# Kernel tuning notes

Measured on AMD Instinct MI355X. Metric: run time of the kernel, lower is better.

Reference implementation:

```python
import jax, jax.numpy as jnp
import numpy as np

# ---- multi-res 4D hash encoding config (Instant-NGP style) ----
L = 16                     # num_levels
T = 2 ** 19                # hash table entries per level (log2_hashmap_size)
FDIM = 2                   # features per entry (input_ch = L*2)
MIN_RES = np.array([16, 16, 16, 16], dtype=np.float64)
MAX_RES = np.array([256, 256, 256, 128], dtype=np.float64)
_growth = (MAX_RES / MIN_RES) ** (1.0 / (L - 1))
RES = np.floor(MIN_RES[None, :] * _growth[None, :] ** np.arange(L)[:, None]).astype(np.int32)  # [L,4]
PRIMES = np.array([1, 2654435761, 805459861, 3674653429], dtype=np.uint32)
# 16 corner offsets of the 4D hypercube
OFFS = np.array([[(c >> d) & 1 for d in range(4)] for c in range(16)], dtype=np.int32)  # [16,4]


def hash_encode(x, table):
    """x: [N,4] in [0,1); table: [L,T,FDIM] -> [N, L*FDIM]."""
    offs = jnp.asarray(OFFS)
    primes = jnp.asarray(PRIMES)
    outs = []
    for l in range(L):  # fixed small loop over levels
        res = jnp.asarray(RES[l], dtype=x.dtype)          # [4]
        pos = x * (res - 1.0)                              # [N,4]
        base = jnp.floor(pos)
        frac = pos - base                                  # [N,4]
        base_i = base.astype(jnp.int32)
        coord = jnp.clip(base_i[:, None, :] + offs[None], 0, jnp.asarray(RES[l] - 1))  # [N,16,4]
        h = coord.astype(jnp.uint32) * primes              # [N,16,4] u32 wraparound mult
        idx = (h[..., 0] ^ h[..., 1] ^ h[..., 2] ^ h[..., 3]) & jnp.uint32(T - 1)      # [N,16]
        feats = table[l][idx.astype(jnp.int32)]            # irregular gather -> [N,16,FDIM]
        # quadrilinear weights: prod over dims of frac / (1-frac)
        w = jnp.prod(jnp.where(offs[None] == 1, frac[:, None, :], 1.0 - frac[:, None, :]), axis=-1)  # [N,16]
        outs.append(jnp.einsum('nc,ncf->nf', w, feats))    # [N,FDIM]
    return jnp.concatenate(outs, axis=-1)                  # [N, L*FDIM]


def setup_inputs() -> dict:
    key = jax.random.key(0)
    ks = jax.random.split(key, 8)
    N = 1048576
    H = 64
    in_ch = L * FDIM  # 32
    x = jax.random.uniform(ks[0], (N, 4), dtype=jnp.float32)
    # NGP hash tables initialized uniform in [-1e-4, 1e-4]
    table = jax.random.uniform(ks[1], (L, T, FDIM), dtype=jnp.float32, minval=-1e-4, maxval=1e-4)
    def lin(k, out_d, in_d):
        b = 1.0 / np.sqrt(in_d)
        return jax.random.uniform(k, (out_d, in_d), dtype=jnp.float32, minval=-b, maxval=b)
    w0 = lin(ks[2], H, in_ch)
    w1 = lin(ks[3], H, H)
    w2 = lin(ks[4], H, H)
    w_out = lin(ks[5], 3, H)
    b_out = jax.random.uniform(ks[6], (3,), dtype=jnp.float32, minval=-1.0/np.sqrt(H), maxval=1.0/np.sqrt(H))
    return {"x": x, "table": table, "w0": w0, "w1": w1, "w2": w2, "w_out": w_out, "b_out": b_out}


def reference(x, table, w0, w1, w2, w_out, b_out):
    h = hash_encode(x, table)                 # [N, 32]
    for W in (w0, w1, w2):                    # bias-free Linear + ReLU x3
        h = jax.nn.relu(h @ W.T)
    v = h @ w_out.T + b_out                   # [N, 3]
    return v
```

## Files before the change

### kernel.cpp

```cpp
#include <hip/hip_runtime.h>
#include <math.h>

#define NLVL  16
#define TSZ   (1u << 19)
#define TMASK (TSZ - 1u)

struct ResArr { int m1[NLVL * 4]; };

typedef short  short8  __attribute__((ext_vector_type(8)));
typedef float  float4v __attribute__((ext_vector_type(4)));

static __device__ __forceinline__ unsigned short f2bf(float f) {
    unsigned u = __float_as_uint(f);
    return (unsigned short)((u + 0x7fffu + ((u >> 16) & 1u)) >> 16);
}

__global__ __launch_bounds__(256)
void cvt_table(const float4* __restrict__ t, uint2* __restrict__ o, int totalPairs)
{
    for (int i = blockIdx.x * 256 + (int)threadIdx.x; i < totalPairs;
         i += gridDim.x * 256) {
        const float4 e = t[i];
        o[i] = make_uint2((unsigned)f2bf(e.x) | ((unsigned)f2bf(e.y) << 16),
                          (unsigned)f2bf(e.z) | ((unsigned)f2bf(e.w) << 16));
    }
}

static __device__ __forceinline__
void encode_point_bf16(const float4*   __restrict__ x,
                       const unsigned* __restrict__ tbl,
                       unsigned*       __restrict__ featbf,
                       int N, int l, int n, const ResArr& res)
{
    if (n >= N) return;

    const float4 xv = x[n];
    const float px[4] = {xv.x, xv.y, xv.z, xv.w};

    int   bi[4];
    float fr[4], om[4];
    #pragma unroll
    for (int d = 0; d < 4; ++d) {
        const int r = res.m1[l * 4 + d];
        const float pos = px[d] * (float)r;
        const float fb  = floorf(pos);
        fr[d] = pos - fb;
        om[d] = 1.0f - fr[d];
        bi[d] = (int)fb;
    }
    const unsigned* tl  = tbl + (size_t)l * TSZ;
    const uint2*    tl2 = (const uint2*)tl;
    const uint4*    tl4 = (const uint4*)tl;

    unsigned hrest[8];
    #pragma unroll
    for (int p = 0; p < 8; ++p) {
        const int c1 = bi[1] + ( p       & 1);
        const int c2 = bi[2] + ((p >> 1) & 1);
        const int c3 = bi[3] + ((p >> 2) & 1);
        hrest[p] = ((unsigned)c1 * 2654435761u)
                 ^ ((unsigned)c2 * 805459861u)
                 ^ ((unsigned)c3 * 3674653429u);
    }

    const int b0 = bi[0];
    unsigned ea[8], eb[8];

    if ((b0 & 1) == 0) {
        #pragma unroll
        for (int p = 0; p < 8; ++p) {
            const unsigned h = ((unsigned)b0 ^ hrest[p]) & TMASK;
            const uint2 q = tl2[h >> 1];
            ea[p] = (h & 1u) ? q.y : q.x;
            eb[p] = (h & 1u) ? q.x : q.y;
        }
    } else if ((b0 & 3) == 1) {
        #pragma unroll
        for (int p = 0; p < 8; ++p) {
            const unsigned hA = ((unsigned)b0 ^ hrest[p]) & TMASK;
            const uint4 q = tl4[hA >> 2];
            const unsigned jA  = hA & 3u;
            const unsigned loA = (jA & 2u) ? q.z : q.x;
            const unsigned hiA = (jA & 2u) ? q.w : q.y;
            const unsigned loB = (jA & 2u) ? q.x : q.z;
            const unsigned hiB = (jA & 2u) ? q.y : q.w;
            ea[p] = (jA & 1u) ? hiA : loA;
            eb[p] = (jA & 1u) ? loB : hiB;
        }
    } else {
        #pragma unroll
        for (int p = 0; p < 8; ++p) {
            const unsigned hA = ((unsigned)b0       ^ hrest[p]) & TMASK;
            const unsigned hB = ((unsigned)(b0 + 1) ^ hrest[p]) & TMASK;
            ea[p] = tl[hA];
            eb[p] = tl[hB];
        }
    }

    float2 fv[16];
    #pragma unroll
    for (int p = 0; p < 8; ++p) {
        fv[2 * p]     = make_float2(__uint_as_float(ea[p] << 16),
                                    __uint_as_float(ea[p] & 0xffff0000u));
        fv[2 * p + 1] = make_float2(__uint_as_float(eb[p] << 16),
                                    __uint_as_float(eb[p] & 0xffff0000u));
    }

    float wt[16];
    #pragma unroll
    for (int c = 0; c < 16; ++c) {
        float w = ( c       & 1) ? fr[0] : om[0];
        w      *= ((c >> 1) & 1) ? fr[1] : om[1];
        w      *= ((c >> 2) & 1) ? fr[2] : om[2];
        w      *= ((c >> 3) & 1) ? fr[3] : om[3];
        wt[c] = w;
    }

    float a0 = 0.0f, a1 = 0.0f;
    #pragma unroll
    for (int c = 0; c < 16; ++c) {
        a0 = fmaf(wt[c], fv[c].x, a0);
        a1 = fmaf(wt[c], fv[c].y, a1);
    }
    featbf[(size_t)l * N + n] = (unsigned)f2bf(a0) | ((unsigned)f2bf(a1) << 16);
}

__global__ __launch_bounds__(256, 4)
void ingp_encode_bf16(const float4*   __restrict__ x,
                      const unsigned* __restrict__ tbl,
                      unsigned*       __restrict__ featbf,
                      int N, int chunksPerLevel, ResArr res)
{
    const int l     = blockIdx.x / chunksPerLevel;
    const int chunk = blockIdx.x - l * chunksPerLevel;
    encode_point_bf16(x, tbl, featbf, N, l, chunk * 256 + (int)threadIdx.x, res);
}

static __device__ __forceinline__
void encode_point_f32(const float4* __restrict__ x,
                      const float2* __restrict__ table,
                      unsigned*     __restrict__ featbf,
                      int N, int l, int n, const ResArr& res)
{
    if (n >= N) return;

    const float4 xv = x[n];
    const float px[4] = {xv.x, xv.y, xv.z, xv.w};

    int   bi[4];
    float fr[4], om[4];
    #pragma unroll
    for (int d = 0; d < 4; ++d) {
        const int r = res.m1[l * 4 + d];
        const float pos = px[d] * (float)r;
        const float fb  = floorf(pos);
        fr[d] = pos - fb;
        om[d] = 1.0f - fr[d];
        bi[d] = (int)fb;
    }
    const float2* tl  = table + (size_t)l * TSZ;
    const float4* tl4 = (const float4*)tl;

    unsigned hrest[8];
    #pragma unroll
    for (int p = 0; p < 8; ++p) {
        const int c1 = bi[1] + ( p       & 1);
        const int c2 = bi[2] + ((p >> 1) & 1);
        const int c3 = bi[3] + ((p >> 2) & 1);
        hrest[p] = ((unsigned)c1 * 2654435761u)
                 ^ ((unsigned)c2 * 805459861u)
                 ^ ((unsigned)c3 * 3674653429u);
    }

    float2 fv[16];
    if ((bi[0] & 1) == 0) {
        #pragma unroll
        for (int p = 0; p < 8; ++p) {
            const unsigned h = ((unsigned)bi[0] ^ hrest[p]) & TMASK;
            const float4 q = tl4[h >> 1];
            const bool odd = (h & 1);
            fv[2 * p]     = odd ? make_float2(q.z, q.w) : make_float2(q.x, q.y);
            fv[2 * p + 1] = odd ? make_float2(q.x, q.y) : make_float2(q.z, q.w);
        }
    } else {
        #pragma unroll
        for (int p = 0; p < 8; ++p) {
            const unsigned hA = ((unsigned)bi[0]       ^ hrest[p]) & TMASK;
            const unsigned hB = ((unsigned)(bi[0] + 1) ^ hrest[p]) & TMASK;
            fv[2 * p]     = tl[hA];
            fv[2 * p + 1] = tl[hB];
        }
    }

    float wt[16];
    #pragma unroll
    for (int c = 0; c < 16; ++c) {
        float w = ( c       & 1) ? fr[0] : om[0];
        w      *= ((c >> 1) & 1) ? fr[1] : om[1];
        w      *= ((c >> 2) & 1) ? fr[2] : om[2];
        w      *= ((c >> 3) & 1) ? fr[3] : om[3];
        wt[c] = w;
    }

    float a0 = 0.0f, a1 = 0.0f;
    #pragma unroll
    for (int c = 0; c < 16; ++c) {
        a0 = fmaf(wt[c], fv[c].x, a0);
        a1 = fmaf(wt[c], fv[c].y, a1);
    }
    featbf[(size_t)l * N + n] = (unsigned)f2bf(a0) | ((unsigned)f2bf(a1) << 16);
}

__global__ __launch_bounds__(256, 4)
void ingp_encode_f32(const float4* __restrict__ x,
                     const float2* __restrict__ table,
                     unsigned*     __restrict__ featbf,
                     int N, int chunksPerLevel, ResArr res)
{
    const int l     = blockIdx.x / chunksPerLevel;
    const int chunk = blockIdx.x - l * chunksPerLevel;
    encode_point_f32(x, table, featbf, N, l, chunk * 256 + (int)threadIdx.x, res);
}

#define TILE_BODY(P0, A0)                                                     \
{                                                                             \
    asm volatile("" : "+v"(idx0));    \
    float4v acc0[4];                                                          \
    _Pragma("unroll")                                                         \
    for (int t = 0; t < 4; ++t) {                                             \
        acc0[t] = (float4v){0.f, 0.f, 0.f, 0.f};                              \
        acc0[t] = __builtin_amdgcn_mfma_f32_16x16x32_bf16(A0, w0f[t], acc0[t], 0, 0, 0); \
    }                                                                         \
    _Pragma("unroll")                                                         \
    for (int t = 0; t < 4; ++t)                                               \
        _Pragma("unroll")                                                     \
        for (int r = 0; r < 4; ++r)                                           \
            *(unsigned short*)(hbase + (q * 4 + r) * 144 + (t * 16 + nn) * 2) = \
                f2bf(fmaxf(acc0[t][r], 0.0f));                                \
    short8 a1[2];                                                             \
    _Pragma("unroll")                                                         \
    for (int s = 0; s < 2; ++s)                                               \
        a1[s] = *(const short8*)(hbase + nn * 144 + s * 64 + q * 16);         \
    float4v acc1[4];                                                          \
    _Pragma("unroll")                                                         \
    for (int t = 0; t < 4; ++t) {                                             \
        acc1[t] = (float4v){0.f, 0.f, 0.f, 0.f};                              \
        _Pragma("unroll")                                                     \
        for (int s = 0; s < 2; ++s)                                           \
            acc1[t] = __builtin_amdgcn_mfma_f32_16x16x32_bf16(a1[s], w1f[s][t], acc1[t], 0, 0, 0); \
    }                                                                         \
    _Pragma("unroll")                                                         \
    for (int t = 0; t < 4; ++t)                                               \
        _Pragma("unroll")                                                     \
        for (int r = 0; r < 4; ++r)                                           \
            *(unsigned short*)(hbase + (q * 4 + r) * 144 + (t * 16 + nn) * 2) = \
                f2bf(fmaxf(acc1[t][r], 0.0f));                                \
    short8 a2[2];                                                             \
    _Pragma("unroll")                                                         \
    for (int s = 0; s < 2; ++s)                                               \
        a2[s] = *(const short8*)(hbase + nn * 144 + s * 64 + q * 16);         \
    float4v acc2[4];                                                          \
    _Pragma("unroll")                                                         \
    for (int t = 0; t < 4; ++t) {                                             \
        acc2[t] = (float4v){0.f, 0.f, 0.f, 0.f};                              \
        _Pragma("unroll")                                                     \
        for (int s = 0; s < 2; ++s) {                                         \
            const short8 w2x = *(const short8*)(wlds + ((12 + s * 4 + t) * 64 + lane) * 16 + idx0); \
            acc2[t] = __builtin_amdgcn_mfma_f32_16x16x32_bf16(a2[s], w2x, acc2[t], 0, 0, 0); \
        }                                                                     \
    }                                                                         \
    _Pragma("unroll")                                                         \
    for (int t = 0; t < 4; ++t)                                               \
        _Pragma("unroll")                                                     \
        for (int r = 0; r < 4; ++r)                                           \
            *(unsigned short*)(hbase + (q * 4 + r) * 144 + (t * 16 + nn) * 2) = \
                f2bf(fmaxf(acc2[t][r], 0.0f));                                \
    short8 a3[2];                                                             \
    _Pragma("unroll")                                                         \
    for (int s = 0; s < 2; ++s)                                               \
        a3[s] = *(const short8*)(hbase + nn * 144 + s * 64 + q * 16);         \
    float4v oc = (float4v){0.f, 0.f, 0.f, 0.f};                               \
    _Pragma("unroll")                                                         \
    for (int s = 0; s < 2; ++s) {                                             \
        const short8 wox = *(const short8*)(wlds + ((20 + s) * 64 + lane) * 16 + idx0); \
        oc = __builtin_amdgcn_mfma_f32_16x16x32_bf16(a3[s], wox, oc, 0, 0, 0); \
    }                                                                         \
    if (nn < 3) {                                                             \
        _Pragma("unroll")                                                     \
        for (int r = 0; r < 4; ++r) {                                         \
            const int pt = (P0) + q * 4 + r;                                  \
            if (pt < N) out[pt * 3 + nn] = oc[r] + bias;                      \
        }                                                                     \
    }                                                                         \
}

static __device__ __forceinline__
void stage_wlds(const float* __restrict__ w0, const float* __restrict__ w1,
                const float* __restrict__ w2, const float* __restrict__ wout,
                char* wlds, int tid)
{
    if (tid < 64) {
        const int lane = tid;
        const int q  = lane >> 4;
        const int nn = lane & 15;
        #pragma unroll
        for (int t = 0; t < 4; ++t) {
            const float* wr = w0 + (t * 16 + nn) * 32 + q * 8;
            short8 f;
            #pragma unroll
            for (int e = 0; e < 8; ++e) f[e] = (short)f2bf(wr[e]);
            *(short8*)(wlds + ((0 + t) * 64 + lane) * 16) = f;
        }
        #pragma unroll
        for (int s = 0; s < 2; ++s)
            #pragma unroll
            for (int t = 0; t < 4; ++t) {
                const float* wr1 = w1 + (t * 16 + nn) * 64 + s * 32 + q * 8;
                const float* wr2 = w2 + (t * 16 + nn) * 64 + s * 32 + q * 8;
                short8 f1, f2;
                #pragma unroll
                for (int e = 0; e < 8; ++e) {
                    f1[e] = (short)f2bf(wr1[e]);
                    f2[e] = (short)f2bf(wr2[e]);
                }
                *(short8*)(wlds + (( 4 + s * 4 + t) * 64 + lane) * 16) = f1;
                *(short8*)(wlds + ((12 + s * 4 + t) * 64 + lane) * 16) = f2;
            }
        #pragma unroll
        for (int s = 0; s < 2; ++s) {
            short8 f;
            #pragma unroll
            for (int e = 0; e < 8; ++e)
                f[e] = (nn < 3) ? (short)f2bf(wout[nn * 64 + s * 32 + q * 8 + e])
                                : (short)0;
            *(short8*)(wlds + ((20 + s) * 64 + lane) * 16) = f;
        }
    }
}

template <int NT>
static __device__ __forceinline__
void mlp_run(const unsigned* __restrict__ featbf,
             const float*    __restrict__ bout,
             float*          __restrict__ out,
             const char* wlds, char* hbase,
             int N, int firstTile, int lane)
{
    const int q  = lane >> 4;
    const int nn = lane & 15;

    short8 w0f[4];
    #pragma unroll
    for (int t = 0; t < 4; ++t)
        w0f[t] = *(const short8*)(wlds + ((0 + t) * 64 + lane) * 16);
    short8 w1f[2][4];
    #pragma unroll
    for (int s = 0; s < 2; ++s)
        #pragma unroll
        for (int t = 0; t < 4; ++t)
            w1f[s][t] = *(const short8*)(wlds + ((4 + s * 4 + t) * 64 + lane) * 16);
    const float bias = (nn < 3) ? bout[nn] : 0.0f;

    int idx0 = 0;

    unsigned ufA[4], ufB[4];
    {
        const int pA = (firstTile * 16 < N) ? (firstTile * 16 + nn) : 0;
        const int pB = ((firstTile + 1) * 16 < N) ? ((firstTile + 1) * 16 + nn) : 0;
        #pragma unroll
        for (int v = 0; v < 4; ++v) {
            ufA[v] = featbf[(size_t)(q * 4 + v) * N + pA];
            ufB[v] = featbf[(size_t)(q * 4 + v) * N + pB];
        }
    }

    for (int it = 0; it < NT; it += 2) {
        const int p0A = (firstTile + it) * 16;
        if (p0A >= N) break;

        short8 a0A;
        #pragma unroll
        for (int v = 0; v < 4; ++v) {
            a0A[2 * v]     = (short)(ufA[v] & 0xffffu);
            a0A[2 * v + 1] = (short)(ufA[v] >> 16);
        }
        {
            const int p0n = (firstTile + it + 2) * 16;
            const bool more = (it + 2 < NT) && (p0n < N);
            const int pn = more ? (p0n + nn) : 0;
            #pragma unroll
            for (int v = 0; v < 4; ++v)
                ufA[v] = featbf[(size_t)(q * 4 + v) * N + pn];
        }
        TILE_BODY(p0A, a0A)

        const int p0B = (firstTile + it + 1) * 16;
        if (p0B < N && it + 1 < NT) {
            short8 a0B;
            #pragma unroll
            for (int v = 0; v < 4; ++v) {
                a0B[2 * v]     = (short)(ufB[v] & 0xffffu);
                a0B[2 * v + 1] = (short)(ufB[v] >> 16);
            }
            {
                const int p0n = (firstTile + it + 3) * 16;
                const bool more = (it + 3 < NT) && (p0n < N);
                const int pn = more ? (p0n + nn) : 0;
                #pragma unroll
                for (int v = 0; v < 4; ++v)
                    ufB[v] = featbf[(size_t)(q * 4 + v) * N + pn];
            }
            TILE_BODY(p0B, a0B)
        }
    }
}

#define TILES_PER_WAVE 16

__global__ __launch_bounds__(256, 4)
void ingp_mlp_mfma(const unsigned* __restrict__ featbf,
                   const float*    __restrict__ w0,
                   const float*    __restrict__ w1,
                   const float*    __restrict__ w2,
                   const float*    __restrict__ wout,
                   const float*    __restrict__ bout,
                   float*          __restrict__ out,
                   int N)
{
    __shared__ char lds_raw[4 * 16 * 144];
    __shared__ char wlds[22 * 64 * 16];

    const int tid = (int)threadIdx.x;
    stage_wlds(w0, w1, w2, wout, wlds, tid);
    __syncthreads();

    const int wave = tid >> 6;
    const int lane = tid & 63;
    char* hbase = lds_raw + wave * (16 * 144);
    mlp_run<TILES_PER_WAVE>(featbf, bout, out, wlds, hbase, N,
                            ((int)blockIdx.x * 4 + wave) * TILES_PER_WAVE, lane);
}

__global__ __launch_bounds__(256, 2)
void ingp_fused(const float4* __restrict__ x,
                const float2* __restrict__ table,
                const float*  __restrict__ w0,
                const float*  __restrict__ w1,
                const float*  __restrict__ w2,
                const float*  __restrict__ wout,
                const float*  __restrict__ bout,
                float*        __restrict__ out,
                int N, ResArr res)
{
    const int n = blockIdx.x * blockDim.x + threadIdx.x;
    if (n >= N) return;

    const float4 xv = x[n];
    const float px[4] = {xv.x, xv.y, xv.z, xv.w};

    float h1[64];
    #pragma unroll
    for (int j = 0; j < 64; ++j) h1[j] = 0.0f;

    float a0p = 0.0f, a1p = 0.0f;

    #pragma unroll 1
    for (int l = 0; l < NLVL; ++l) {
        int   rm[4], bi[4];
        float fr[4], om[4];
        #pragma unroll
        for (int d = 0; d < 4; ++d) {
            const int r = res.m1[l * 4 + d];
            rm[d] = r;
            const float pos = px[d] * (float)r;
            const float fb  = floorf(pos);
            fr[d] = pos - fb;
            om[d] = 1.0f - fr[d];
            bi[d] = (int)fb;
        }
        const float2* tl = table + (size_t)l * TSZ;

        float2 fv[16];
        float  wt[16];
        #pragma unroll
        for (int c = 0; c < 16; ++c) {
            int c0 = bi[0] + ( c       & 1);
            int c1 = bi[1] + ((c >> 1) & 1);
            int c2 = bi[2] + ((c >> 2) & 1);
            int c3 = bi[3] + ((c >> 3) & 1);
            c0 = min(max(c0, 0), rm[0]);
            c1 = min(max(c1, 0), rm[1]);
            c2 = min(max(c2, 0), rm[2]);
            c3 = min(max(c3, 0), rm[3]);
            const unsigned hh = (unsigned)c0
                              ^ ((unsigned)c1 * 2654435761u)
                              ^ ((unsigned)c2 * 805459861u)
                              ^ ((unsigned)c3 * 3674653429u);
            fv[c] = tl[hh & TMASK];
            float w = ( c       & 1) ? fr[0] : om[0];
            w      *= ((c >> 1) & 1) ? fr[1] : om[1];
            w      *= ((c >> 2) & 1) ? fr[2] : om[2];
            w      *= ((c >> 3) & 1) ? fr[3] : om[3];
            wt[c] = w;
        }
        {
            const int lp = (l == 0) ? 0 : (l - 1);
            const float* w0c = w0 + 2 * lp;
            #pragma unroll
            for (int j = 0; j < 64; ++j)
                h1[j] = fmaf(w0c[j * 32], a0p, fmaf(w0c[j * 32 + 1], a1p, h1[j]));
        }
        float a0 = 0.0f, a1 = 0.0f;
        #pragma unroll
        for (int c = 0; c < 16; ++c) {
            a0 = fmaf(wt[c], fv[c].x, a0);
            a1 = fmaf(wt[c], fv[c].y, a1);
        }
        a0p = a0; a1p = a1;
    }
    {
        const float* w0c = w0 + 2 * (NLVL - 1);
        #pragma unroll
        for (int j = 0; j < 64; ++j)
            h1[j] = fmaf(w0c[j * 32], a0p, fmaf(w0c[j * 32 + 1], a1p, h1[j]));
    }
    #pragma unroll
    for (int j = 0; j < 64; ++j) h1[j] = fmaxf(h1[j], 0.0f);

    float h2[64];
    #pragma unroll
    for (int j = 0; j < 64; ++j) {
        float acc = 0.0f;
        const float* wr = w1 + j * 64;
        #pragma unroll
        for (int i = 0; i < 64; ++i) acc = fmaf(wr[i], h1[i], acc);
        h2[j] = fmaxf(acc, 0.0f);
    }
    float h3[64];
    #pragma unroll
    for (int j = 0; j < 64; ++j) {
        float acc = 0.0f;
        const float* wr = w2 + j * 64;
        #pragma unroll
        for (int i = 0; i < 64; ++i) acc = fmaf(wr[i], h2[i], acc);
        h3[j] = fmaxf(acc, 0.0f);
    }
    float o[3];
    #pragma unroll
    for (int k = 0; k < 3; ++k) {
        float acc = bout[k];
        const float* wr = wout + k * 64;
        #pragma unroll
        for (int i = 0; i < 64; ++i) acc = fmaf(wr[i], h3[i], acc);
        o[k] = acc;
    }
    out[n * 3 + 0] = o[0];
    out[n * 3 + 1] = o[1];
    out[n * 3 + 2] = o[2];
}

extern "C" void kernel_launch(void* const* d_in, const int* in_sizes, int n_in,
                              void* d_out, int out_size, void* d_ws, size_t ws_size,
                              hipStream_t stream) {
    (void)n_in; (void)out_size;

    const float* x     = (const float*)d_in[0];
    const float* table = (const float*)d_in[1];
    const float* w0    = (const float*)d_in[2];
    const float* w1    = (const float*)d_in[3];
    const float* w2    = (const float*)d_in[4];
    const float* wout  = (const float*)d_in[5];
    const float* bout  = (const float*)d_in[6];
    float* out = (float*)d_out;

    const int N = in_sizes[0] / 4;

    ResArr res;
    for (int d = 0; d < 4; ++d) {
        const double minr = 16.0;
        const double maxr = (d == 3) ? 128.0 : 256.0;
        const double growth = pow(maxr / minr, 1.0 / (double)(NLVL - 1));
        for (int l = 0; l < NLVL; ++l) {
            const int r = (int)floor(minr * pow(growth, (double)l));
            res.m1[l * 4 + d] = r - 1;
        }
    }

    const size_t tblBytes  = (size_t)NLVL * TSZ * sizeof(unsigned);
    const size_t featBytes = (size_t)NLVL * (size_t)N * sizeof(unsigned);
    const int chunksPerLevel = (N + 255) / 256;

    const int tiles  = (N + 15) / 16;
    const int waves  = (tiles + TILES_PER_WAVE - 1) / TILES_PER_WAVE;
    const int blocks = (waves + 3) / 4;

    if (ws_size >= tblBytes + featBytes) {
        unsigned* tblbf  = (unsigned*)d_ws;
        unsigned* featbf = (unsigned*)((char*)d_ws + tblBytes);

        hipLaunchKernelGGL(cvt_table, dim3(2048), dim3(256), 0, stream,
                           (const float4*)table, (uint2*)tblbf,
                           (int)(NLVL * TSZ / 2));

        hipLaunchKernelGGL(ingp_encode_bf16, dim3(NLVL * chunksPerLevel), dim3(256),
                           0, stream, (const float4*)x, tblbf,
                           featbf, N, chunksPerLevel, res);

        hipLaunchKernelGGL(ingp_mlp_mfma, dim3(blocks), dim3(256), 0, stream,
                           featbf, w0, w1, w2, wout, bout, out, N);
    } else if (ws_size >= featBytes) {
        unsigned* featbf = (unsigned*)d_ws;
        hipLaunchKernelGGL(ingp_encode_f32, dim3(NLVL * chunksPerLevel), dim3(256),
                           0, stream, (const float4*)x, (const float2*)table,
                           featbf, N, chunksPerLevel, res);

        hipLaunchKernelGGL(ingp_mlp_mfma, dim3(blocks), dim3(256), 0, stream,
                           featbf, w0, w1, w2, wout, bout, out, N);
    } else {
        hipLaunchKernelGGL(ingp_fused, dim3((N + 255) / 256), dim3(256), 0, stream,
                           (const float4*)x, (const float2*)table,
                           w0, w1, w2, wout, bout, out, N, res);
    }
}
```

Measured before the change: 704.3 us.

## Merge table conversion and encoding into one cooperative persistent kernel

Replaces the separate bf16 table-conversion launch and the encode launch with a single cooperative kernel. The kernel converts the table, does a grid-wide sync, then runs the encode units in a grid-stride persistent loop. This removes one kernel launch and the gap between the two kernels. In exchange the grid is capped at 2048 blocks, which reduces parallelism for the gather-heavy encode, and it adds the cost of a grid barrier. It falls back to the two-kernel path if a cooperative launch is not available.

Result: slower. 1.154 ms (+63.8%).

```diff
diff --git a/kernel.cpp b/kernel.cpp
--- a/kernel.cpp
+++ b/kernel.cpp
@@ -1,5 +1,8 @@
 #include <hip/hip_runtime.h>
+#include <hip/hip_cooperative_groups.h>
 #include <math.h>
+
+namespace cg = cooperative_groups;
 
 #define NLVL  16
 #define TSZ   (1u << 19)
@@ -13,6 +16,134 @@
 static __device__ __forceinline__ unsigned short f2bf(float f) {
     unsigned u = __float_as_uint(f);
     return (unsigned short)((u + 0x7fffu + ((u >> 16) & 1u)) >> 16);
+}
+
+static __device__ __forceinline__
+void encode_point_bf16(const float4*   __restrict__ x,
+                       const unsigned* __restrict__ tbl,
+                       unsigned*       __restrict__ featbf,
+                       int N, int l, int n, const ResArr& res)
+{
+    if (n < N) {
+        const float4 xv = x[n];
+        const float px[4] = {xv.x, xv.y, xv.z, xv.w};
+
+        int   bi[4];
+        float fr[4], om[4];
+        #pragma unroll
+        for (int d = 0; d < 4; ++d) {
+            const int r = res.m1[l * 4 + d];
+            const float pos = px[d] * (float)r;
+            const float fb  = floorf(pos);
+            fr[d] = pos - fb;
+            om[d] = 1.0f - fr[d];
+            bi[d] = (int)fb;
+        }
+        const unsigned* tl  = tbl + (size_t)l * TSZ;
+        const uint2*    tl2 = (const uint2*)tl;
+        const uint4*    tl4 = (const uint4*)tl;
+
+        unsigned hrest[8];
+        #pragma unroll
+        for (int p = 0; p < 8; ++p) {
+            const int c1 = bi[1] + ( p       & 1);
+            const int c2 = bi[2] + ((p >> 1) & 1);
+            const int c3 = bi[3] + ((p >> 2) & 1);
+            hrest[p] = ((unsigned)c1 * 2654435761u)
+                     ^ ((unsigned)c2 * 805459861u)
+                     ^ ((unsigned)c3 * 3674653429u);
+        }
+
+        const int b0 = bi[0];
+        unsigned ea[8], eb[8];
+
+        if ((b0 & 1) == 0) {
+            #pragma unroll
+            for (int p = 0; p < 8; ++p) {
+                const unsigned h = ((unsigned)b0 ^ hrest[p]) & TMASK;
+                const uint2 q = tl2[h >> 1];
+                ea[p] = (h & 1u) ? q.y : q.x;
+                eb[p] = (h & 1u) ? q.x : q.y;
+            }
+        } else if ((b0 & 3) == 1) {
+            #pragma unroll
+            for (int p = 0; p < 8; ++p) {
+                const unsigned hA = ((unsigned)b0 ^ hrest[p]) & TMASK;
+                const uint4 q = tl4[hA >> 2];
+                const unsigned jA  = hA & 3u;
+                const unsigned loA = (jA & 2u) ? q.z : q.x;
+                const unsigned hiA = (jA & 2u) ? q.w : q.y;
+                const unsigned loB = (jA & 2u) ? q.x : q.z;
+                const unsigned hiB = (jA & 2u) ? q.y : q.w;
+                ea[p] = (jA & 1u) ? hiA : loA;
+                eb[p] = (jA & 1u) ? loB : hiB;
+            }
+        } else {
+            #pragma unroll
+            for (int p = 0; p < 8; ++p) {
+                const unsigned hA = ((unsigned)b0       ^ hrest[p]) & TMASK;
+                const unsigned hB = ((unsigned)(b0 + 1) ^ hrest[p]) & TMASK;
+                ea[p] = tl[hA];
+                eb[p] = tl[hB];
+            }
+        }
+
+        float2 fv[16];
+        #pragma unroll
+        for (int p = 0; p < 8; ++p) {
+            fv[2 * p]     = make_float2(__uint_as_float(ea[p] << 16),
+                                        __uint_as_float(ea[p] & 0xffff0000u));
+            fv[2 * p + 1] = make_float2(__uint_as_float(eb[p] << 16),
+                                        __uint_as_float(eb[p] & 0xffff0000u));
+        }
+
+        float wt[16];
+        #pragma unroll
+        for (int c = 0; c < 16; ++c) {
+            float w = ( c       & 1) ? fr[0] : om[0];
+            w      *= ((c >> 1) & 1) ? fr[1] : om[1];
+            w      *= ((c >> 2) & 1) ? fr[2] : om[2];
+            w      *= ((c >> 3) & 1) ? fr[3] : om[3];
+            wt[c] = w;
+        }
+
+        float a0 = 0.0f, a1 = 0.0f;
+        #pragma unroll
+        for (int c = 0; c < 16; ++c) {
+            a0 = fmaf(wt[c], fv[c].x, a0);
+            a1 = fmaf(wt[c], fv[c].y, a1);
+        }
+        featbf[(size_t)l * N + n] = (unsigned)f2bf(a0) | ((unsigned)f2bf(a1) << 16);
+    }
+}
+
+__global__ __launch_bounds__(256, 8)
+void ingp_cvt_encode(const float4*   __restrict__ x,
+                     const float4*   __restrict__ table4,
+                     unsigned*       __restrict__ tblbf,
+                     unsigned*       __restrict__ featbf,
+                     int N, int chunksPerLevel, int totalUnits, ResArr res)
+{
+    const int tid = (int)threadIdx.x;
+    const int gsz = (int)gridDim.x * 256;
+
+    {
+        uint2* o = (uint2*)tblbf;
+        const int totalPairs = (int)(NLVL * TSZ / 2);
+        for (int i = (int)blockIdx.x * 256 + tid; i < totalPairs; i += gsz) {
+            const float4 e = table4[i];
+            o[i] = make_uint2((unsigned)f2bf(e.x) | ((unsigned)f2bf(e.y) << 16),
+                              (unsigned)f2bf(e.z) | ((unsigned)f2bf(e.w) << 16));
+        }
+    }
+    __threadfence();
+    cg::this_grid().sync();
+
+    for (int u = (int)blockIdx.x; u < totalUnits; u += (int)gridDim.x) {
+        const int l     = u / chunksPerLevel;
+        const int chunk = u - l * chunksPerLevel;
+        encode_point_bf16(x, tblbf, featbf, N, l, chunk * 256 + tid, res);
+    }
 }
 
 __global__ __launch_bounds__(256)
@@ -24,105 +155,6 @@
         o[i] = make_uint2((unsigned)f2bf(e.x) | ((unsigned)f2bf(e.y) << 16),
                           (unsigned)f2bf(e.z) | ((unsigned)f2bf(e.w) << 16));
     }
-}
-
-static __device__ __forceinline__
-void encode_point_bf16(const float4*   __restrict__ x,
-                       const unsigned* __restrict__ tbl,
-                       unsigned*       __restrict__ featbf,
-                       int N, int l, int n, const ResArr& res)
-{
-    if (n >= N) return;
-
-    const float4 xv = x[n];
-    const float px[4] = {xv.x, xv.y, xv.z, xv.w};
-
-    int   bi[4];
-    float fr[4], om[4];
-    #pragma unroll
-    for (int d = 0; d < 4; ++d) {
-        const int r = res.m1[l * 4 + d];
-        const float pos = px[d] * (float)r;
-        const float fb  = floorf(pos);
-        fr[d] = pos - fb;
-        om[d] = 1.0f - fr[d];
-        bi[d] = (int)fb;
-    }
-    const unsigned* tl  = tbl + (size_t)l * TSZ;
-    const uint2*    tl2 = (const uint2*)tl;
-    const uint4*    tl4 = (const uint4*)tl;
-
-    unsigned hrest[8];
-    #pragma unroll
-    for (int p = 0; p < 8; ++p) {
-        const int c1 = bi[1] + ( p       & 1);
-        const int c2 = bi[2] + ((p >> 1) & 1);
-        const int c3 = bi[3] + ((p >> 2) & 1);
-        hrest[p] = ((unsigned)c1 * 2654435761u)
-                 ^ ((unsigned)c2 * 805459861u)
-                 ^ ((unsigned)c3 * 3674653429u);
-    }
-
-    const int b0 = bi[0];
-    unsigned ea[8], eb[8];
-
-    if ((b0 & 1) == 0) {
-        #pragma unroll
-        for (int p = 0; p < 8; ++p) {
-            const unsigned h = ((unsigned)b0 ^ hrest[p]) & TMASK;
-            const uint2 q = tl2[h >> 1];
-            ea[p] = (h & 1u) ? q.y : q.x;
-            eb[p] = (h & 1u) ? q.x : q.y;
-        }
-    } else if ((b0 & 3) == 1) {
-        #pragma unroll
-        for (int p = 0; p < 8; ++p) {
-            const unsigned hA = ((unsigned)b0 ^ hrest[p]) & TMASK;
-            const uint4 q = tl4[hA >> 2];
-            const unsigned jA  = hA & 3u;
-            const unsigned loA = (jA & 2u) ? q.z : q.x;
-            const unsigned hiA = (jA & 2u) ? q.w : q.y;
-            const unsigned loB = (jA & 2u) ? q.x : q.z;
-            const unsigned hiB = (jA & 2u) ? q.y : q.w;
-            ea[p] = (jA & 1u) ? hiA : loA;
-            eb[p] = (jA & 1u) ? loB : hiB;
-        }
-    } else {
-        #pragma unroll
-        for (int p = 0; p < 8; ++p) {
-            const unsigned hA = ((unsigned)b0       ^ hrest[p]) & TMASK;
-            const unsigned hB = ((unsigned)(b0 + 1) ^ hrest[p]) & TMASK;
-            ea[p] = tl[hA];
-            eb[p] = tl[hB];
-        }
-    }
-
-    float2 fv[16];
-    #pragma unroll
-    for (int p = 0; p < 8; ++p) {
-        fv[2 * p]     = make_float2(__uint_as_float(ea[p] << 16),
-                                    __uint_as_float(ea[p] & 0xffff0000u));
-        fv[2 * p + 1] = make_float2(__uint_as_float(eb[p] << 16),
-                                    __uint_as_float(eb[p] & 0xffff0000u));
-    }
-
-    float wt[16];
-    #pragma unroll
-    for (int c = 0; c < 16; ++c) {
-        float w = ( c       & 1) ? fr[0] : om[0];
-        w      *= ((c >> 1) & 1) ? fr[1] : om[1];
-        w      *= ((c >> 2) & 1) ? fr[2] : om[2];
-        w      *= ((c >> 3) & 1) ? fr[3] : om[3];
-        wt[c] = w;
-    }
-
-    float a0 = 0.0f, a1 = 0.0f;
-    #pragma unroll
-    for (int c = 0; c < 16; ++c) {
-        a0 = fmaf(wt[c], fv[c].x, a0);
-        a1 = fmaf(wt[c], fv[c].y, a1);
-    }
-    featbf[(size_t)l * N + n] = (unsigned)f2bf(a0) | ((unsigned)f2bf(a1) << 16);
 }
 
 __global__ __launch_bounds__(256, 4)
@@ -589,28 +621,62 @@
     const size_t tblBytes  = (size_t)NLVL * TSZ * sizeof(unsigned);
     const size_t featBytes = (size_t)NLVL * (size_t)N * sizeof(unsigned);
     const int chunksPerLevel = (N + 255) / 256;
+    const int totalUnits     = NLVL * chunksPerLevel;
 
     const int tiles  = (N + 15) / 16;
     const int waves  = (tiles + TILES_PER_WAVE - 1) / TILES_PER_WAVE;
     const int blocks = (waves + 3) / 4;
 
+    static int s_coopGrid = -2;
+    if (s_coopGrid == -2) {
+        s_coopGrid = 0;
+        hipDeviceProp_t prop;
+        if (hipGetDeviceProperties(&prop, 0) == hipSuccess && prop.cooperativeLaunch) {
+            int maxB = 0;
+            if (hipOccupancyMaxActiveBlocksPerMultiprocessor(
+                    &maxB, (const void*)ingp_cvt_encode, 256, 0) == hipSuccess &&
+                maxB > 0) {
+                long long cap = (long long)maxB * prop.multiProcessorCount;
+                if (cap > 2048) cap = 2048;
+                s_coopGrid = (int)cap;
+            }
+        }
+    }
+
     if (ws_size >= tblBytes + featBytes) {
         unsigned* tblbf  = (unsigned*)d_ws;
         unsigned* featbf = (unsigned*)((char*)d_ws + tblBytes);
 
-        hipLaunchKernelGGL(cvt_table, dim3(2048), dim3(256), 0, stream,
-                           (const float4*)table, (uint2*)tblbf,
-                           (int)(NLVL * TSZ / 2));
-
-        hipLaunchKernelGGL(ingp_encode_bf16, dim3(NLVL * chunksPerLevel), dim3(256),
-                           0, stream, (const float4*)x, tblbf,
-                           featbf, N, chunksPerLevel, res);
+        bool launched = false;
+        if (s_coopGrid > 0) {
+            const float4* x4 = (const float4*)x;
+            const float4* t4 = (const float4*)table;
+            int N_ = N, cpl_ = chunksPerLevel, tu_ = totalUnits;
+            void* args[] = { (void*)&x4, (void*)&t4, (void*)&tblbf, (void*)&featbf,
+                             (void*)&N_, (void*)&cpl_, (void*)&tu_, (void*)&res };
+            hipError_t err = hipLaunchCooperativeKernel(
+                (const void*)ingp_cvt_encode, dim3(s_coopGrid), dim3(256),
+                args, 0, stream);
+            if (err == hipSuccess) {
+                launched = true;
+            } else {
+                s_coopGrid = 0;
+            }
+        }
+        if (!launched) {
+            hipLaunchKernelGGL(cvt_table, dim3(2048), dim3(256), 0, stream,
+                               (const float4*)table, (uint2*)tblbf,
+                               (int)(NLVL * TSZ / 2));
+            hipLaunchKernelGGL(ingp_encode_bf16, dim3(totalUnits), dim3(256),
+                               0, stream, (const float4*)x, tblbf,
+                               featbf, N, chunksPerLevel, res);
+        }
 
         hipLaunchKernelGGL(ingp_mlp_mfma, dim3(blocks), dim3(256), 0, stream,
                            featbf, w0, w1, w2, wout, bout, out, N);
     } else if (ws_size >= featBytes) {
         unsigned* featbf = (unsigned*)d_ws;
-        hipLaunchKernelGGL(ingp_encode_f32, dim3(NLVL * chunksPerLevel), dim3(256),
+        hipLaunchKernelGGL(ingp_encode_f32, dim3(totalUnits), dim3(256),
                            0, stream, (const float4*)x, (const float2*)table,
                            featbf, N, chunksPerLevel, res);
 
```
